# Kernel tuning notes

Hardware: AMD Instinct MI355X
Metric: run time of the kernel (lower is better)

## Reference

```python
import jax, jax.numpy as jnp
import numpy as np

N_HEADS = 4
D_K = 64

def setup_inputs() -> dict:
    key = jax.random.key(0)
    k1, k2, k3 = jax.random.split(key, 3)
    B, C, H, W = 16, 256, 32, 32
    x = jax.random.normal(k1, (B, C, H, W), dtype=jnp.float32)
    # Linear(C, 3*n_heads*d_k) stored as [in, out] for x @ W
    w_proj = jax.random.normal(k2, (C, 3 * N_HEADS * D_K), dtype=jnp.float32) * (1.0 / np.sqrt(C))
    b_proj = jnp.zeros((3 * N_HEADS * D_K,), dtype=jnp.float32)
    w_out = jax.random.normal(k3, (N_HEADS * D_K, C), dtype=jnp.float32) * (1.0 / np.sqrt(N_HEADS * D_K))
    b_out = jnp.zeros((C,), dtype=jnp.float32)
    return {"x": x, "w_proj": w_proj, "b_proj": b_proj, "w_out": w_out, "b_out": b_out}

def reference(x, w_proj, b_proj, w_out, b_out):
    B, C, H, W = x.shape
    S = H * W
    scale = D_K ** -0.5
    xs = x.reshape(B, C, S).transpose(0, 2, 1)            # [B, S, C]
    qkv = (xs @ w_proj + b_proj).reshape(B, S, N_HEADS, 3 * D_K)
    q, k, v = jnp.split(qkv, 3, axis=3)                    # each [B, S, H, dk]
    attn = jnp.einsum('bihd,bjhd->bijh', q, k) * scale     # [B, S, S, heads]
    attn = jax.nn.softmax(attn, axis=2)
    o = jnp.einsum('bijh,bjhd->bihd', attn, v)             # [B, S, heads, dk]
    o = o.reshape(B, S, N_HEADS * D_K)
    res = o @ w_out + b_out + xs                           # [B, S, C]
    return res.transpose(0, 2, 1).reshape(B, C, H, W)
```

## Files before the change

### kernel.cpp

```cpp
#include <hip/hip_runtime.h>
#include <math.h>

#define B_  16
#define C_  256
#define S_  1024
#define NH  4
#define DK  64
#define P3  768
#define ND  256

typedef unsigned short u16;
typedef unsigned int   u32;
typedef float  f32x4  __attribute__((ext_vector_type(4)));
typedef short  bf16x8 __attribute__((ext_vector_type(8)));

#define MFMA16(a, b, c) __builtin_amdgcn_mfma_f32_16x16x32_bf16(a, b, c, 0, 0, 0)

#define QSCALE 0.1803368801111137f

__device__ __forceinline__ u16 f2bf(float f) {
    union { float f; u32 u; } x; x.f = f;
    u32 r = x.u + 0x7fffu + ((x.u >> 16) & 1u);
    return (u16)(r >> 16);
}

__device__ __forceinline__ void stage16(const u16* g, u16* l) {
    __builtin_amdgcn_global_load_lds(
        (const __attribute__((address_space(1))) void*)g,
        (__attribute__((address_space(3))) void*)l, 16, 0, 0);
}

__global__ __launch_bounds__(256) void transpose_cvt(
    const float* __restrict__ src, u16* __restrict__ dst, int R, int Cc)
{
    __shared__ float T[64][65];
    const int tid = threadIdx.x;
    const int c0 = blockIdx.x * 64, r0 = blockIdx.y * 64, z = blockIdx.z;
    src += (size_t)z * R * Cc;
    dst += (size_t)z * R * Cc;

    const int l64 = tid & 63, rr0 = tid >> 6;
    #pragma unroll
    for (int t = 0; t < 16; ++t) {
        int rr = rr0 + t * 4;
        T[rr][l64] = src[(size_t)(r0 + rr) * Cc + c0 + l64];
    }
    __syncthreads();
    const int rp = tid & 31;
    const int cb = tid >> 5;
    #pragma unroll
    for (int t = 0; t < 8; ++t) {
        int c = cb + t * 8;
        u32 lo = f2bf(T[2 * rp][c]);
        u32 hi = f2bf(T[2 * rp + 1][c]);
        *(u32*)&dst[(size_t)(c0 + c) * R + r0 + 2 * rp] = lo | (hi << 16);
    }
}

__global__ __launch_bounds__(256) void transpose_w(
    const float* __restrict__ wp, u16* __restrict__ wpT,
    const float* __restrict__ wo, u16* __restrict__ woT)
{
    const int z = blockIdx.z;
    const int Cc = z ? 256 : 768;
    if ((int)blockIdx.x * 64 >= Cc) return;
    const float* src = z ? wo : wp;
    u16* dst = z ? woT : wpT;
    const int R = 256;

    __shared__ float T[64][65];
    const int tid = threadIdx.x;
    const int c0 = blockIdx.x * 64, r0 = blockIdx.y * 64;

    const int l64 = tid & 63, rr0 = tid >> 6;
    #pragma unroll
    for (int t = 0; t < 16; ++t) {
        int rr = rr0 + t * 4;
        T[rr][l64] = src[(size_t)(r0 + rr) * Cc + c0 + l64];
    }
    __syncthreads();
    const int rp = tid & 31;
    const int cb = tid >> 5;
    #pragma unroll
    for (int t = 0; t < 8; ++t) {
        int c = cb + t * 8;
        u32 lo = f2bf(T[2 * rp][c]);
        u32 hi = f2bf(T[2 * rp + 1][c]);
        *(u32*)&dst[(size_t)(c0 + c) * R + r0 + 2 * rp] = lo | (hi << 16);
    }
}

__global__ __launch_bounds__(256) void qkv_mfma(
    const u16* __restrict__ xt, const u16* __restrict__ wpT,
    const float* __restrict__ bp, u16* __restrict__ qo,
    u16* __restrict__ ko, u16* __restrict__ vo)
{
    __shared__ __align__(16) u16 SM[24576];
    u16* As = SM;
    u16* Bs = SM + 16384;

    const int tid = threadIdx.x;
    const int w = tid >> 6, lane = tid & 63;
    const int n_ = lane & 15, quad = lane >> 4;

    const int id = blockIdx.x;
    const int xcd = id & 7, g = id >> 3;
    const int n0 = (g % 12) * 64;
    const int sb = xcd * 16 + g / 12;
    const int s0 = (sb & 7) * 128, b = sb >> 3;

    const u16* ar0 = xt + ((size_t)b * S_ + s0 + (2 * w + 0) * 16 + n_) * C_ + quad * 8;
    const u16* ar1 = xt + ((size_t)b * S_ + s0 + (2 * w + 1) * 16 + n_) * C_ + quad * 8;
    const u16* br  = wpT + (size_t)(n0 + w * 16 + n_) * C_ + quad * 8;

    f32x4 acc[2][4];
    #pragma unroll
    for (int am = 0; am < 2; ++am)
        #pragma unroll
        for (int nf = 0; nf < 4; ++nf)
            #pragma unroll
            for (int r = 0; r < 4; ++r) acc[am][nf][r] = 0.f;

    #pragma unroll
    for (int kb = 0; kb < 2; ++kb) {
        const int kcb = kb * 128;
        __syncthreads();
        #pragma unroll
        for (int kc = 0; kc < 4; ++kc) {
            stage16(ar0 + kcb + kc * 32, As + ((2 * w + 0) * 4 + kc) * 512);
            stage16(ar1 + kcb + kc * 32, As + ((2 * w + 1) * 4 + kc) * 512);
            stage16(br  + kcb + kc * 32, Bs + (w * 4 + kc) * 512);
        }
        __syncthreads();
        #pragma unroll
        for (int kc = 0; kc < 4; ++kc) {
            bf16x8 af0 = *(const bf16x8*)&As[((2 * w + 0) * 4 + kc) * 512 + lane * 8];
            bf16x8 af1 = *(const bf16x8*)&As[((2 * w + 1) * 4 + kc) * 512 + lane * 8];
            #pragma unroll
            for (int nf = 0; nf < 4; ++nf) {
                bf16x8 bf = *(const bf16x8*)&Bs[(nf * 4 + kc) * 512 + lane * 8];
                acc[0][nf] = MFMA16(af0, bf, acc[0][nf]);
                acc[1][nf] = MFMA16(af1, bf, acc[1][nf]);
            }
        }
    }

    const int hd = n0 / 192, rem = n0 % 192, which = rem / 64;
    const int bh = b * NH + hd;
    float bias[4];
    #pragma unroll
    for (int nf = 0; nf < 4; ++nf) bias[nf] = bp[n0 + nf * 16 + n_];
    const float sc = (which == 0) ? QSCALE : 1.f;

    __syncthreads();
    if (which < 2) {
        u16* Cs = SM;
        #pragma unroll
        for (int am = 0; am < 2; ++am) {
            int row0 = w * 32 + am * 16 + quad * 4;
            #pragma unroll
            for (int nf = 0; nf < 4; ++nf)
                #pragma unroll
                for (int r = 0; r < 4; ++r)
                    Cs[(row0 + r) * 72 + nf * 16 + n_] =
                        f2bf((acc[am][nf][r] + bias[nf]) * sc);
        }
        __syncthreads();
        u16* dst = (which == 0) ? qo : ko;
        #pragma unroll
        for (int t = 0; t < 4; ++t) {
            int ii = tid + t * 256;
            int row = ii >> 3, c8 = (ii & 7) * 8;
            *(bf16x8*)&dst[((size_t)bh * S_ + s0 + row) * DK + c8] =
                *(const bf16x8*)&Cs[row * 72 + c8];
        }
    } else {
        u16* Cs = SM;
        #pragma unroll
        for (int am = 0; am < 2; ++am) {
            int colb = w * 32 + am * 16 + quad * 4;
            #pragma unroll
            for (int nf = 0; nf < 4; ++nf)
                #pragma unroll
                for (int r = 0; r < 4; ++r)
                    Cs[(nf * 16 + n_) * 136 + colb + r] =
                        f2bf(acc[am][nf][r] + bias[nf]);
        }
        __syncthreads();
        #pragma unroll
        for (int t = 0; t < 4; ++t) {
            int ii = tid + t * 256;
            int row = ii >> 4, c8 = (ii & 15) * 8;
            *(bf16x8*)&vo[((size_t)bh * DK + row) * S_ + s0 + c8] =
                *(const bf16x8*)&Cs[row * 136 + c8];
        }
    }
}

__global__ __launch_bounds__(256) void attn_mfma(
    const u16* __restrict__ q, const u16* __restrict__ k,
    const u16* __restrict__ vt, u16* __restrict__ obf)
{
    __shared__ __align__(16) u16 SM[16384];
    u16* Ks = SM;
    u16* Vs = SM + 8192;

    const int tid = threadIdx.x;
    const int w = tid >> 6, lane = tid & 63;
    const int n_ = lane & 15, quad = lane >> 4;

    const int id = blockIdx.x;
    const int xcd = id & 7, g = id >> 3;
    const int i0 = (g % 8) * 128;
    const int bh = xcd * 8 + g / 8;
    const int hd = bh & 3, b = bh >> 2;

    bf16x8 qf[2][2];
    #pragma unroll
    for (int am = 0; am < 2; ++am) {
        const u16* qrow = q + ((size_t)bh * S_ + i0 + w * 32 + am * 16 + n_) * DK;
        qf[am][0] = *(const bf16x8*)&qrow[quad * 8];
        qf[am][1] = *(const bf16x8*)&qrow[32 + quad * 8];
    }

    const int k0 = 32 * w + 8 * (n_ >> 2) + (n_ & 3);
    const u16* kb0 = k + ((size_t)bh * S_ + k0) * DK + quad * 8;
    const u16* kb1 = kb0 + 4 * DK;
    const u16* vb  = vt + ((size_t)bh * DK + w * 16 + n_) * S_ + quad * 8;

    float lsum[2] = {0.f, 0.f};
    f32x4 oacc[2][4];
    #pragma unroll
    for (int am = 0; am < 2; ++am)
        #pragma unroll
        for (int nd = 0; nd < 4; ++nd)
            #pragma unroll
            for (int r = 0; r < 4; ++r) oacc[am][nd][r] = 0.f;

    for (int jt = 0; jt < S_; jt += 128) {
        __syncthreads();
        stage16(kb0 + (size_t)jt * DK,      Ks + (2 * w + 0) * 1024);
        stage16(kb0 + (size_t)jt * DK + 32, Ks + (2 * w + 0) * 1024 + 512);
        stage16(kb1 + (size_t)jt * DK,      Ks + (2 * w + 1) * 1024);
        stage16(kb1 + (size_t)jt * DK + 32, Ks + (2 * w + 1) * 1024 + 512);
        #pragma unroll
        for (int mf = 0; mf < 4; ++mf)
            stage16(vb + jt + mf * 32, Vs + (w * 4 + mf) * 512);
        __syncthreads();

        f32x4 sb[2][8];
        #pragma unroll
        for (int nb = 0; nb < 8; ++nb) {
            bf16x8 kf0 = *(const bf16x8*)&Ks[nb * 1024 + lane * 8];
            bf16x8 kf1 = *(const bf16x8*)&Ks[nb * 1024 + 512 + lane * 8];
            #pragma unroll
            for (int am = 0; am < 2; ++am) {
                f32x4 a; a[0] = a[1] = a[2] = a[3] = 0.f;
                a = MFMA16(kf0, qf[am][0], a);
                a = MFMA16(kf1, qf[am][1], a);
                sb[am][nb] = a;
            }
        }

        bf16x8 pa[2][4];
        #pragma unroll
        for (int am = 0; am < 2; ++am) {
            u32 tr[8][4];
            #pragma unroll
            for (int nb = 0; nb < 8; ++nb)
                #pragma unroll
                for (int r = 0; r < 4; ++r) {
                    float p = exp2f(sb[am][nb][r]);
                    u32 bits = __float_as_uint(p) & 0xffff0000u;
                    lsum[am] += __uint_as_float(bits);
                    tr[nb][r] = bits;
                }
            #pragma unroll
            for (int mf = 0; mf < 4; ++mf) {
                union { bf16x8 v; u32 u[4]; } pk;
                pk.u[0] = (tr[2 * mf][0] >> 16) | tr[2 * mf][1];
                pk.u[1] = (tr[2 * mf][2] >> 16) | tr[2 * mf][3];
                pk.u[2] = (tr[2 * mf + 1][0] >> 16) | tr[2 * mf + 1][1];
                pk.u[3] = (tr[2 * mf + 1][2] >> 16) | tr[2 * mf + 1][3];
                pa[am][mf] = pk.v;
            }
        }

        #pragma unroll
        for (int nd = 0; nd < 4; ++nd)
            #pragma unroll
            for (int mf = 0; mf < 4; ++mf) {
                bf16x8 vf = *(const bf16x8*)&Vs[(nd * 4 + mf) * 512 + lane * 8];
                #pragma unroll
                for (int am = 0; am < 2; ++am)
                    oacc[am][nd] = MFMA16(vf, pa[am][mf], oacc[am][nd]);
            }
    }

    float inv[2];
    #pragma unroll
    for (int am = 0; am < 2; ++am) {
        float s = lsum[am];
        s += __shfl_xor(s, 16);
        s += __shfl_xor(s, 32);
        inv[am] = 1.f / s;
    }

    __syncthreads();
    u16* eb = SM + w * 2304;
    #pragma unroll
    for (int am = 0; am < 2; ++am)
        #pragma unroll
        for (int nd = 0; nd < 4; ++nd) {
            uint2 uv;
            uv.x = (u32)f2bf(oacc[am][nd][0] * inv[am]) |
                   ((u32)f2bf(oacc[am][nd][1] * inv[am]) << 16);
            uv.y = (u32)f2bf(oacc[am][nd][2] * inv[am]) |
                   ((u32)f2bf(oacc[am][nd][3] * inv[am]) << 16);
            *(uint2*)&eb[(am * 16 + n_) * 72 + nd * 16 + quad * 4] = uv;
        }
    __syncthreads();
    #pragma unroll
    for (int t = 0; t < 4; ++t) {
        int ii = lane + t * 64;
        int row = ii >> 3, c8 = (ii & 7) * 8;
        *(bf16x8*)&obf[((size_t)b * S_ + i0 + w * 32 + row) * ND + hd * DK + c8] =
            *(const bf16x8*)&eb[row * 72 + c8];
    }
}

__global__ __launch_bounds__(256) void out_proj_mfma(
    const u16* __restrict__ obf, const u16* __restrict__ woT,
    const float* __restrict__ bo, const float* __restrict__ x,
    float* __restrict__ out)
{
    __shared__ __align__(16) u16 SM[24576];
    u16* Bs = SM;
    u16* As = SM + 16384;

    const int tid = threadIdx.x;
    const int w = tid >> 6, lane = tid & 63;
    const int n_ = lane & 15, quad = lane >> 4;

    const int id = blockIdx.x;
    const int xcd = id & 7, g = id >> 3;
    const int c0 = (g % 4) * 64;
    const int sbi = xcd * 16 + g / 4;
    const int s0 = (sbi & 7) * 128, b = sbi >> 3;

    const u16* ar  = woT + (size_t)(c0 + w * 16 + n_) * ND + quad * 8;
    const u16* br0 = obf + ((size_t)b * S_ + s0 + (2 * w + 0) * 16 + n_) * ND + quad * 8;
    const u16* br1 = obf + ((size_t)b * S_ + s0 + (2 * w + 1) * 16 + n_) * ND + quad * 8;

    f32x4 acc[2][4];
    #pragma unroll
    for (int nf = 0; nf < 2; ++nf)
        #pragma unroll
        for (int mb = 0; mb < 4; ++mb)
            #pragma unroll
            for (int r = 0; r < 4; ++r) acc[nf][mb][r] = 0.f;

    #pragma unroll
    for (int kb = 0; kb < 2; ++kb) {
        const int kcb = kb * 128;
        __syncthreads();
        #pragma unroll
        for (int kc = 0; kc < 4; ++kc) {
            stage16(ar  + kcb + kc * 32, As + (w * 4 + kc) * 512);
            stage16(br0 + kcb + kc * 32, Bs + ((2 * w + 0) * 4 + kc) * 512);
            stage16(br1 + kcb + kc * 32, Bs + ((2 * w + 1) * 4 + kc) * 512);
        }
        __syncthreads();
        #pragma unroll
        for (int kc = 0; kc < 4; ++kc) {
            bf16x8 bf0 = *(const bf16x8*)&Bs[((2 * w + 0) * 4 + kc) * 512 + lane * 8];
            bf16x8 bf1 = *(const bf16x8*)&Bs[((2 * w + 1) * 4 + kc) * 512 + lane * 8];
            #pragma unroll
            for (int mb = 0; mb < 4; ++mb) {
                bf16x8 af = *(const bf16x8*)&As[(mb * 4 + kc) * 512 + lane * 8];
                acc[0][mb] = MFMA16(af, bf0, acc[0][mb]);
                acc[1][mb] = MFMA16(af, bf1, acc[1][mb]);
            }
        }
    }

    #pragma unroll
    for (int mb = 0; mb < 4; ++mb)
        #pragma unroll
        for (int r = 0; r < 4; ++r) {
            int c = c0 + mb * 16 + quad * 4 + r;
            float bias = bo[c];
            #pragma unroll
            for (int nf = 0; nf < 2; ++nf) {
                size_t idx = ((size_t)b * C_ + c) * S_ + s0 + w * 32 + nf * 16 + n_;
                out[idx] = acc[nf][mb][r] + bias + x[idx];
            }
        }
}

extern "C" void kernel_launch(void* const* d_in, const int* in_sizes, int n_in,
                              void* d_out, int out_size, void* d_ws, size_t ws_size,
                              hipStream_t stream) {
    const float* x  = (const float*)d_in[0];
    const float* wp = (const float*)d_in[1];
    const float* bp = (const float*)d_in[2];
    const float* wo = (const float*)d_in[3];
    const float* bo = (const float*)d_in[4];
    float* out = (float*)d_out;

    const size_t QKV_E = (size_t)B_ * NH * S_ * DK;
    u16* q   = (u16*)d_ws;
    u16* kk  = q   + QKV_E;
    u16* vtp = kk  + QKV_E;
    u16* obf = vtp + QKV_E;
    u16* xt  = obf + (size_t)B_ * S_ * ND;
    u16* wpT = xt  + (size_t)B_ * S_ * C_;
    u16* woT = wpT + (size_t)P3 * C_;

    transpose_cvt<<<dim3(S_ / 64, C_ / 64, B_), 256, 0, stream>>>(x, xt, C_, S_);
    transpose_w  <<<dim3(12, 4, 2),             256, 0, stream>>>(wp, wpT, wo, woT);
    qkv_mfma     <<<dim3(1536), 256, 0, stream>>>(xt, wpT, bp, q, kk, vtp);
    attn_mfma    <<<dim3(512),  256, 0, stream>>>(q, kk, vtp, obf);
    out_proj_mfma<<<dim3(512),  256, 0, stream>>>(obf, woT, bo, x, out);
}
```

Measured before the change: 150.5 us.

## Split attention keys across waves and reduce partial outputs in shared memory

Each block now handles 32 queries instead of 128, and its four waves each take a quarter of the key range (split-K). Every wave loads K and V fragments straight from global memory into registers, with no LDS staging and no per-tile barriers. The partial outputs and row sums are then combined through shared memory before normalizing and writing bf16. The grid grows to 2048 blocks for more parallelism, at the cost of each K/V tile being read by four times as many blocks and a final cross-wave reduction. The softmax still uses no max subtraction, as before.

```diff
diff --git a/kernel.cpp b/kernel.cpp
--- a/kernel.cpp
+++ b/kernel.cpp
@@ -201,9 +201,8 @@
     const u16* __restrict__ q, const u16* __restrict__ k,
     const u16* __restrict__ vt, u16* __restrict__ obf)
 {
-    __shared__ __align__(16) u16 SM[16384];
-    u16* Ks = SM;
-    u16* Vs = SM + 8192;
+    __shared__ __align__(16) float Lo[4][32][68];
+    __shared__ float Ls[4][32];
 
     const int tid = threadIdx.x;
     const int w = tid >> 6, lane = tid & 63;
@@ -211,22 +210,21 @@
 
     const int id = blockIdx.x;
     const int xcd = id & 7, g = id >> 3;
-    const int i0 = (g % 8) * 128;
-    const int bh = xcd * 8 + g / 8;
+    const int i0 = (g & 31) * 32;
+    const int bh = xcd * 8 + (g >> 5);
     const int hd = bh & 3, b = bh >> 2;
 
     bf16x8 qf[2][2];
     #pragma unroll
     for (int am = 0; am < 2; ++am) {
-        const u16* qrow = q + ((size_t)bh * S_ + i0 + w * 32 + am * 16 + n_) * DK;
+        const u16* qrow = q + ((size_t)bh * S_ + i0 + am * 16 + n_) * DK;
         qf[am][0] = *(const bf16x8*)&qrow[quad * 8];
         qf[am][1] = *(const bf16x8*)&qrow[32 + quad * 8];
     }
 
-    const int k0 = 32 * w + 8 * (n_ >> 2) + (n_ & 3);
-    const u16* kb0 = k + ((size_t)bh * S_ + k0) * DK + quad * 8;
-    const u16* kb1 = kb0 + 4 * DK;
-    const u16* vb  = vt + ((size_t)bh * DK + w * 16 + n_) * S_ + quad * 8;
+    const u16* kbase = k  + (size_t)bh * S_ * DK + quad * 8;
+    const u16* vbase = vt + (size_t)bh * DK * S_ + quad * 8;
+    const int krow = 8 * (n_ >> 2) + (n_ & 3);
 
     float lsum[2] = {0.f, 0.f};
     f32x4 oacc[2][4];
@@ -237,96 +235,93 @@
             #pragma unroll
             for (int r = 0; r < 4; ++r) oacc[am][nd][r] = 0.f;
 
-    for (int jt = 0; jt < S_; jt += 128) {
-        __syncthreads();
-        stage16(kb0 + (size_t)jt * DK,      Ks + (2 * w + 0) * 1024);
-        stage16(kb0 + (size_t)jt * DK + 32, Ks + (2 * w + 0) * 1024 + 512);
-        stage16(kb1 + (size_t)jt * DK,      Ks + (2 * w + 1) * 1024);
-        stage16(kb1 + (size_t)jt * DK + 32, Ks + (2 * w + 1) * 1024 + 512);
-        #pragma unroll
-        for (int mf = 0; mf < 4; ++mf)
-            stage16(vb + jt + mf * 32, Vs + (w * 4 + mf) * 512);
-        __syncthreads();
-
-        f32x4 sb[2][8];
-        #pragma unroll
-        for (int nb = 0; nb < 8; ++nb) {
-            bf16x8 kf0 = *(const bf16x8*)&Ks[nb * 1024 + lane * 8];
-            bf16x8 kf1 = *(const bf16x8*)&Ks[nb * 1024 + 512 + lane * 8];
+    const int keybase = w * 256;
+    #pragma unroll
+    for (int t = 0; t < 8; ++t) {
+        const int kb = keybase + t * 32;
+
+        bf16x8 kf[2][2];
+        #pragma unroll
+        for (int nb = 0; nb < 2; ++nb) {
+            const u16* kp = kbase + (size_t)(kb + krow + 4 * nb) * DK;
+            kf[nb][0] = *(const bf16x8*)&kp[0];
+            kf[nb][1] = *(const bf16x8*)&kp[32];
+        }
+        bf16x8 vf[4];
+        #pragma unroll
+        for (int nd = 0; nd < 4; ++nd)
+            vf[nd] = *(const bf16x8*)&vbase[(size_t)(nd * 16 + n_) * S_ + kb];
+
+        f32x4 sb[2][2];
+        #pragma unroll
+        for (int nb = 0; nb < 2; ++nb)
             #pragma unroll
             for (int am = 0; am < 2; ++am) {
                 f32x4 a; a[0] = a[1] = a[2] = a[3] = 0.f;
-                a = MFMA16(kf0, qf[am][0], a);
-                a = MFMA16(kf1, qf[am][1], a);
+                a = MFMA16(kf[nb][0], qf[am][0], a);
+                a = MFMA16(kf[nb][1], qf[am][1], a);
                 sb[am][nb] = a;
             }
-        }
-
-        bf16x8 pa[2][4];
+
         #pragma unroll
         for (int am = 0; am < 2; ++am) {
-            u32 tr[8][4];
-            #pragma unroll
-            for (int nb = 0; nb < 8; ++nb)
+            u32 bb[2][4];
+            #pragma unroll
+            for (int nb = 0; nb < 2; ++nb)
                 #pragma unroll
                 for (int r = 0; r < 4; ++r) {
                     float p = exp2f(sb[am][nb][r]);
                     u32 bits = __float_as_uint(p) & 0xffff0000u;
                     lsum[am] += __uint_as_float(bits);
-                    tr[nb][r] = bits;
+                    bb[nb][r] = bits;
                 }
-            #pragma unroll
-            for (int mf = 0; mf < 4; ++mf) {
-                union { bf16x8 v; u32 u[4]; } pk;
-                pk.u[0] = (tr[2 * mf][0] >> 16) | tr[2 * mf][1];
-                pk.u[1] = (tr[2 * mf][2] >> 16) | tr[2 * mf][3];
-                pk.u[2] = (tr[2 * mf + 1][0] >> 16) | tr[2 * mf + 1][1];
-                pk.u[3] = (tr[2 * mf + 1][2] >> 16) | tr[2 * mf + 1][3];
-                pa[am][mf] = pk.v;
-            }
-        }
-
-        #pragma unroll
-        for (int nd = 0; nd < 4; ++nd)
-            #pragma unroll
-            for (int mf = 0; mf < 4; ++mf) {
-                bf16x8 vf = *(const bf16x8*)&Vs[(nd * 4 + mf) * 512 + lane * 8];
-                #pragma unroll
-                for (int am = 0; am < 2; ++am)
-                    oacc[am][nd] = MFMA16(vf, pa[am][mf], oacc[am][nd]);
-            }
-    }
-
-    float inv[2];
+            union { bf16x8 v; u32 u[4]; } pk;
+            pk.u[0] = (bb[0][0] >> 16) | bb[0][1];
+            pk.u[1] = (bb[0][2] >> 16) | bb[0][3];
+            pk.u[2] = (bb[1][0] >> 16) | bb[1][1];
+            pk.u[3] = (bb[1][2] >> 16) | bb[1][3];
+            #pragma unroll
+            for (int nd = 0; nd < 4; ++nd)
+                oacc[am][nd] = MFMA16(vf[nd], pk.v, oacc[am][nd]);
+        }
+    }
+
+    float ws[2];
     #pragma unroll
     for (int am = 0; am < 2; ++am) {
         float s = lsum[am];
         s += __shfl_xor(s, 16);
         s += __shfl_xor(s, 32);
-        inv[am] = 1.f / s;
-    }
-
+        ws[am] = s;
+    }
+    if (quad == 0) {
+        Ls[w][n_]      = ws[0];
+        Ls[w][16 + n_] = ws[1];
+    }
+    #pragma unroll
+    for (int am = 0; am < 2; ++am)
+        #pragma unroll
+        for (int nd = 0; nd < 4; ++nd)
+            *(f32x4*)&Lo[w][am * 16 + n_][nd * 16 + quad * 4] = oacc[am][nd];
     __syncthreads();
-    u16* eb = SM + w * 2304;
-    #pragma unroll
-    for (int am = 0; am < 2; ++am)
-        #pragma unroll
-        for (int nd = 0; nd < 4; ++nd) {
-            uint2 uv;
-            uv.x = (u32)f2bf(oacc[am][nd][0] * inv[am]) |
-                   ((u32)f2bf(oacc[am][nd][1] * inv[am]) << 16);
-            uv.y = (u32)f2bf(oacc[am][nd][2] * inv[am]) |
-                   ((u32)f2bf(oacc[am][nd][3] * inv[am]) << 16);
-            *(uint2*)&eb[(am * 16 + n_) * 72 + nd * 16 + quad * 4] = uv;
-        }
-    __syncthreads();
-    #pragma unroll
-    for (int t = 0; t < 4; ++t) {
-        int ii = lane + t * 64;
-        int row = ii >> 3, c8 = (ii & 7) * 8;
-        *(bf16x8*)&obf[((size_t)b * S_ + i0 + w * 32 + row) * ND + hd * DK + c8] =
-            *(const bf16x8*)&eb[row * 72 + c8];
-    }
+
+    const int qq = tid >> 3, d0 = (tid & 7) * 8;
+    f32x4 a0 = *(const f32x4*)&Lo[0][qq][d0];
+    f32x4 a1 = *(const f32x4*)&Lo[0][qq][d0 + 4];
+    #pragma unroll
+    for (int wv = 1; wv < 4; ++wv) {
+        f32x4 b0 = *(const f32x4*)&Lo[wv][qq][d0];
+        f32x4 b1 = *(const f32x4*)&Lo[wv][qq][d0 + 4];
+        #pragma unroll
+        for (int r = 0; r < 4; ++r) { a0[r] += b0[r]; a1[r] += b1[r]; }
+    }
+    const float inv = 1.f / (Ls[0][qq] + Ls[1][qq] + Ls[2][qq] + Ls[3][qq]);
+    union { bf16x8 v; u32 u[4]; } ov;
+    ov.u[0] = (u32)f2bf(a0[0] * inv) | ((u32)f2bf(a0[1] * inv) << 16);
+    ov.u[1] = (u32)f2bf(a0[2] * inv) | ((u32)f2bf(a0[3] * inv) << 16);
+    ov.u[2] = (u32)f2bf(a1[0] * inv) | ((u32)f2bf(a1[1] * inv) << 16);
+    ov.u[3] = (u32)f2bf(a1[2] * inv) | ((u32)f2bf(a1[3] * inv) << 16);
+    *(bf16x8*)&obf[((size_t)b * S_ + i0 + qq) * ND + hd * DK + d0] = ov.v;
 }
 
 __global__ __launch_bounds__(256) void out_proj_mfma(
@@ -420,6 +415,6 @@
     transpose_cvt<<<dim3(S_ / 64, C_ / 64, B_), 256, 0, stream>>>(x, xt, C_, S_);
     transpose_w  <<<dim3(12, 4, 2),             256, 0, stream>>>(wp, wpT, wo, woT);
     qkv_mfma     <<<dim3(1536), 256, 0, stream>>>(xt, wpT, bp, q, kk, vtp);
-    attn_mfma    <<<dim3(512),  256, 0, stream>>>(q, kk, vtp, obf);
+    attn_mfma    <<<dim3(2048), 256, 0, stream>>>(q, kk, vtp, obf);
     out_proj_mfma<<<dim3(512),  256, 0, stream>>>(obf, woT, bo, x, out);
 }
```

Result: slower. 175.8 us (+16.8%).
